# Performance work log

Measured on AMD Instinct MI355X. Metric: run time of the kernel, lower is better.

Reference implementation:

```python
import jax, jax.numpy as jnp
import numpy as np

EPS = 1e-5
NEG_SLOPE = 0.01  # torch leaky_relu default


def _layer_norm(x, g, b):
    m = jnp.mean(x, axis=-1, keepdims=True)
    v = jnp.var(x, axis=-1, keepdims=True)
    return (x - m) * jax.lax.rsqrt(v + EPS) * g + b


def setup_inputs() -> dict:
    key = jax.random.key(0)
    ks = jax.random.split(key, 8)
    bs, n, c, out_c, enc_dim = 8, 2048, 128, 128, 64
    s = 1.0 / np.sqrt(c)
    return {
        "x": jax.random.normal(ks[0], (bs, n, c), jnp.float32),
        "enc": jax.random.normal(ks[1], (bs, n, enc_dim), jnp.float32),
        "W_enc": jax.random.uniform(ks[2], (c, enc_dim), jnp.float32, -1, 1) / np.sqrt(enc_dim),
        "b_enc": jnp.zeros((c,), jnp.float32),
        "g1": jnp.ones((c,), jnp.float32),
        "b1": jnp.zeros((c,), jnp.float32),
        "g2": jnp.ones((c,), jnp.float32),
        "b2": jnp.zeros((c,), jnp.float32),
        "W0": jax.random.uniform(ks[3], (c, c), jnp.float32, -1, 1) * s,
        "Wa": jax.random.uniform(ks[4], (2 * c,), jnp.float32, -1, 1) / np.sqrt(2 * c),
        "W1": jax.random.uniform(ks[5], (out_c, c), jnp.float32, -1, 1) * s,
    }


def reference(x, enc, W_enc, b_enc, g1, b1, g2, b2, W0, Wa, W1):
    c = x.shape[-1]
    k = 1
    # positional encoding projection
    x = x + enc @ W_enc.T + b_enc
    x_norm = _layer_norm(x, g1, b1)
    # head i=0 (k=1)
    h = x_norm @ W0.T  # [bs, n, c]
    # GAT attention: e[b,i,j] = leaky_relu(a . cat(h_i, h_j)) computed via split weights
    a1, a2 = Wa[:c], Wa[c:]
    s1 = h @ a1  # [bs, n] contribution of node i
    s2 = h @ a2  # [bs, n] contribution of node j
    e = jax.nn.leaky_relu(s1[:, :, None] + s2[:, None, :], NEG_SLOPE)  # [bs, n, n]
    atten = jax.nn.softmax(e, axis=2)
    attentioned = jnp.einsum("bij,bjc->bic", atten, h)
    attentioned = attentioned + x  # residual
    attentioned = _layer_norm(attentioned, g2, b2)
    h_next = jax.nn.elu(attentioned @ W1.T) / k
    atten_agg = jax.lax.stop_gradient(atten) / k
    return h_next, atten_agg
```

## Files before the change

### kernel.cpp

```cpp
#include <hip/hip_runtime.h>
#include <hip/hip_bf16.h>
#include <cstddef>

#define EPS 1e-5f
#define NSLOPE 0.01f
#define L2E 1.44269504f

typedef __attribute__((ext_vector_type(8))) short s16x8;
typedef __attribute__((ext_vector_type(4))) float f32x4;

union BF8 { unsigned short u[8]; s16x8 v; };

static __device__ inline unsigned short f2bf(float f) {
    unsigned int u = __float_as_uint(f);
    u += 0x7fffu + ((u >> 16) & 1u);
    return (unsigned short)(u >> 16);
}

static __device__ inline void nt_store4(float* p, f32x4 v) {
    __builtin_nontemporal_store(v, (f32x4*)p);
}

__global__ __launch_bounds__(256) void kW(
    const float* __restrict__ W_enc, const float* __restrict__ W0,
    const float* __restrict__ W1,
    unsigned short* __restrict__ Web, unsigned short* __restrict__ W0b,
    unsigned short* __restrict__ W1b)
{
    int idx = blockIdx.x * 256 + threadIdx.x;
    if (idx < 128 * 64) Web[idx] = f2bf(W_enc[idx]);
    if (idx < 128 * 128) { W0b[idx] = f2bf(W0[idx]); W1b[idx] = f2bf(W1[idx]); }
}

__global__ __launch_bounds__(256, 4) void kA(
    const float* __restrict__ x, const float* __restrict__ enc,
    const unsigned short* __restrict__ Web, const float* __restrict__ b_enc,
    const float* __restrict__ g1, const float* __restrict__ b1,
    const unsigned short* __restrict__ W0b, const float* __restrict__ Wa,
    float* __restrict__ xnew, unsigned short* __restrict__ hP,
    float* __restrict__ s1, float* __restrict__ s2)
{
    __shared__ float ys[32][132];
    __shared__ unsigned short xnb[32][136];
    __shared__ unsigned short hts[128][40];
    __shared__ float ps1[2][32], ps2[2][32];

    int t = threadIdx.x;
    int w = t >> 6, lane = t & 63;
    int ml = lane & 15, quad = lane >> 4;
    int mrow = (w & 1) * 16;
    int chalf = (w >> 1) * 64;
    long long R0 = (long long)blockIdx.x * 32;
    int b = (int)(R0 >> 11);
    int jt = (int)((R0 & 2047) >> 5);

    f32x4 acc1[4] = {};
    const float* encrow = enc + (R0 + mrow + ml) * 64 + quad * 8;
#pragma unroll
    for (int kb = 0; kb < 2; ++kb) {
        float4 e0 = *(const float4*)(encrow + kb * 32);
        float4 e1 = *(const float4*)(encrow + kb * 32 + 4);
        BF8 af;
        af.u[0] = f2bf(e0.x); af.u[1] = f2bf(e0.y);
        af.u[2] = f2bf(e0.z); af.u[3] = f2bf(e0.w);
        af.u[4] = f2bf(e1.x); af.u[5] = f2bf(e1.y);
        af.u[6] = f2bf(e1.z); af.u[7] = f2bf(e1.w);
#pragma unroll
        for (int ct = 0; ct < 4; ++ct) {
            int n = chalf + ct * 16 + ml;
            s16x8 bf = *(const s16x8*)(Web + n * 64 + kb * 32 + quad * 8);
            acc1[ct] = __builtin_amdgcn_mfma_f32_16x16x32_bf16(af.v, bf, acc1[ct], 0, 0, 0);
        }
    }
#pragma unroll
    for (int ct = 0; ct < 4; ++ct) {
        int col = chalf + ct * 16 + ml;
        float be = b_enc[col];
#pragma unroll
        for (int rg = 0; rg < 4; ++rg) {
            int rl = mrow + quad * 4 + rg;
            long long row = R0 + rl;
            float y = acc1[ct][rg] + x[row * 128 + col] + be;
            xnew[row * 128 + col] = y;
            ys[rl][col] = y;
        }
    }
    __syncthreads();

    {
        int rl = t >> 3, sub = t & 7;
        float v[16];
        float s = 0.f, q = 0.f;
#pragma unroll
        for (int i = 0; i < 16; ++i) {
            v[i] = ys[rl][sub * 16 + i];
            s += v[i]; q += v[i] * v[i];
        }
#pragma unroll
        for (int m = 1; m < 8; m <<= 1) { s += __shfl_xor(s, m); q += __shfl_xor(q, m); }
        float mean = s * (1.f / 128.f);
        float var = q * (1.f / 128.f) - mean * mean;
        float rstd = rsqrtf(var + EPS);
#pragma unroll
        for (int i = 0; i < 16; ++i) {
            int col = sub * 16 + i;
            float xn = (v[i] - mean) * rstd * g1[col] + b1[col];
            xnb[rl][col] = f2bf(xn);
        }
    }
    __syncthreads();

    f32x4 acc2[4] = {};
#pragma unroll
    for (int kb = 0; kb < 4; ++kb) {
        s16x8 af = *(const s16x8*)(&xnb[mrow + ml][kb * 32 + quad * 8]);
#pragma unroll
        for (int ct = 0; ct < 4; ++ct) {
            int n = chalf + ct * 16 + ml;
            s16x8 bf = *(const s16x8*)(W0b + n * 128 + kb * 32 + quad * 8);
            acc2[ct] = __builtin_amdgcn_mfma_f32_16x16x32_bf16(af, bf, acc2[ct], 0, 0, 0);
        }
    }

#pragma unroll
    for (int ct = 0; ct < 4; ++ct) {
        int col = chalf + ct * 16 + ml;
#pragma unroll
        for (int rg = 0; rg < 4; ++rg)
            hts[col][mrow + quad * 4 + rg] = f2bf(acc2[ct][rg]);
    }
#pragma unroll
    for (int rg = 0; rg < 4; ++rg) {
        float p1 = 0.f, p2 = 0.f;
#pragma unroll
        for (int ct = 0; ct < 4; ++ct) {
            int col = chalf + ct * 16 + ml;
            p1 += acc2[ct][rg] * Wa[col];
            p2 += acc2[ct][rg] * Wa[128 + col];
        }
#pragma unroll
        for (int m = 1; m < 16; m <<= 1) { p1 += __shfl_xor(p1, m); p2 += __shfl_xor(p2, m); }
        if (ml == 0) {
            int rl = mrow + quad * 4 + rg;
            ps1[w >> 1][rl] = p1;
            ps2[w >> 1][rl] = p2;
        }
    }
    __syncthreads();
    if (t < 32) {
        s1[R0 + t] = ps1[0][t] + ps1[1][t];
        s2[R0 + t] = ps2[0][t] + ps2[1][t];
    }
    {
        int c = t >> 1, half = t & 1;
        unsigned short* dst = hP + (((long long)b * 64 + jt) * 128 + c) * 32 + half * 16;
        const unsigned short* srcp = &hts[c][half * 16];
        *(s16x8*)(dst) = *(const s16x8*)(srcp);
        *(s16x8*)(dst + 8) = *(const s16x8*)(srcp + 8);
    }
}

__global__ __launch_bounds__(1024) void kC(
    const float* __restrict__ s1, const float* __restrict__ s2,
    float* __restrict__ Crow)
{
    __shared__ float t[2048], ph[2048], pl[2048];
    __shared__ float wmax[16];
    __shared__ float M2sh;
    int tid = threadIdx.x;
    int b = blockIdx.x;
    const float* s2b = s2 + b * 2048;

    float m = -1e30f;
    for (int i = tid; i < 2048; i += 1024) {
        float v = s2b[i];
        t[i] = v;
        m = fmaxf(m, v);
    }
#pragma unroll
    for (int d = 32; d; d >>= 1) m = fmaxf(m, __shfl_xor(m, d));
    if ((tid & 63) == 0) wmax[tid >> 6] = m;
    __syncthreads();
    if (tid == 0) {
        float mm = wmax[0];
#pragma unroll
        for (int i = 1; i < 16; ++i) mm = fmaxf(mm, wmax[i]);
        M2sh = mm;
    }
    __syncthreads();
    float M2 = M2sh;

    for (int k = 2; k <= 2048; k <<= 1) {
        for (int j = k >> 1; j > 0; j >>= 1) {
            for (int i = tid; i < 2048; i += 1024) {
                int ixj = i ^ j;
                if (ixj > i) {
                    float a = t[i], c = t[ixj];
                    bool up = ((i & k) == 0);
                    if ((a > c) == up) { t[i] = c; t[ixj] = a; }
                }
            }
            __syncthreads();
        }
    }

    if (tid < 64) {
        int base = tid * 32;
        float ch = 0.f, cl = 0.f;
        for (int q = 0; q < 32; ++q) {
            float d = t[base + q] - M2;
            ch += __expf(d);           ph[base + q] = ch;
            cl += __expf(NSLOPE * d);  pl[base + q] = cl;
        }
        float sh = ch, sl = cl;
#pragma unroll
        for (int d = 1; d < 64; d <<= 1) {
            float uh = __shfl_up(sh, d);
            float ul = __shfl_up(sl, d);
            if (tid >= d) { sh += uh; sl += ul; }
        }
        float offh = sh - ch, offl = sl - cl;
        for (int q = 0; q < 32; ++q) { ph[base + q] += offh; pl[base + q] += offl; }
    }
    __syncthreads();

    float tot_hi = ph[2047];
    for (int r = tid; r < 2048; r += 1024) {
        float s1i = s1[b * 2048 + r];
        float zc = -s1i;
        int lo = 0, hi = 2048;
#pragma unroll
        for (int it = 0; it < 11; ++it) {
            int mid = (lo + hi) >> 1;
            if (t[mid] < zc) lo = mid + 1; else hi = mid;
        }
        float sum_hi = tot_hi - (lo > 0 ? ph[lo - 1] : 0.f);
        float sum_lo = (lo > 0 ? pl[lo - 1] : 0.f);
        float z0 = s1i + M2;
        float mi = fmaxf(z0, NSLOPE * z0);
        float A = __expf(z0 - mi);
        float B = __expf(NSLOPE * z0 - mi);
        Crow[b * 2048 + r] = mi + __logf(A * sum_hi + B * sum_lo);
    }
}

__global__ __launch_bounds__(256, 4) void kD(
    const float* __restrict__ s1, const float* __restrict__ s2,
    const float* __restrict__ Crow, const unsigned short* __restrict__ hP,
    float* __restrict__ atten, float* __restrict__ attn)
{
    __shared__ float Pt[4][16][36];
    __shared__ float Rbuf[3][16][132];

    int t = threadIdx.x;
    int w = t >> 6, lane = t & 63;
    int bid = blockIdx.x;
    int swz = (bid & 7) * 128 + (bid >> 3);
    int b = swz >> 7;
    int it = swz & 127;
    int i0 = it * 16;
    int ml = lane & 15, quad = lane >> 4;

    const float* s2b = s2 + (long long)b * 2048;

    float s1i  = s1[(long long)b * 2048 + i0 + ml];
    float CiL2 = Crow[(long long)b * 2048 + i0 + ml] * L2E;
    const unsigned short* hPb = hP + (long long)b * 64 * 128 * 32;
    int sr = lane >> 3, sc = lane & 7;
    float* abase = atten + ((long long)b * 2048 + i0) * 2048;

    f32x4 acc[8] = {};
    for (int jj = 0; jj < 512; jj += 32) {
        int j0 = w * 512 + jj;
        int jb = j0 + quad * 8;
        float4 sa = *(const float4*)(s2b + jb);
        float4 sb = *(const float4*)(s2b + jb + 4);
        float zs[8] = {sa.x, sa.y, sa.z, sa.w, sb.x, sb.y, sb.z, sb.w};
        float p[8];
        BF8 af;
#pragma unroll
        for (int k = 0; k < 8; ++k) {
            float z = s1i + zs[k];
            float zl = fmaxf(z, NSLOPE * z);
            p[k] = exp2f(fmaf(zl, L2E, -CiL2));
            af.u[k] = f2bf(p[k]);
        }
        *(f32x4*)&Pt[w][ml][quad * 8]     = *(const f32x4*)&p[0];
        *(f32x4*)&Pt[w][ml][quad * 8 + 4] = *(const f32x4*)&p[4];
        f32x4 r0 = *(const f32x4*)&Pt[w][sr][sc * 4];
        f32x4 r1 = *(const f32x4*)&Pt[w][8 + sr][sc * 4];
        nt_store4(abase + (long long)sr * 2048 + j0 + sc * 4, r0);
        nt_store4(abase + (long long)(8 + sr) * 2048 + j0 + sc * 4, r1);

        const unsigned short* tb = hPb + (long long)(j0 >> 5) * 128 * 32;
#pragma unroll
        for (int ct = 0; ct < 8; ++ct) {
            s16x8 bfrag = *(const s16x8*)(tb + (ct * 16 + ml) * 32 + quad * 8);
            acc[ct] = __builtin_amdgcn_mfma_f32_16x16x32_bf16(af.v, bfrag, acc[ct], 0, 0, 0);
        }
    }

    if (w > 0) {
#pragma unroll
        for (int ct = 0; ct < 8; ++ct)
#pragma unroll
            for (int rg = 0; rg < 4; ++rg)
                Rbuf[w - 1][quad * 4 + rg][ct * 16 + ml] = acc[ct][rg];
    }
    __syncthreads();
    if (w == 0) {
#pragma unroll
        for (int ct = 0; ct < 8; ++ct) {
#pragma unroll
            for (int rg = 0; rg < 4; ++rg) {
                int ii = quad * 4 + rg;
                int cc = ct * 16 + ml;
                float v = acc[ct][rg] + Rbuf[0][ii][cc] + Rbuf[1][ii][cc]
                        + Rbuf[2][ii][cc];
                attn[((long long)b * 2048 + i0 + ii) * 128 + cc] = v;
            }
        }
    }
}

__global__ __launch_bounds__(256, 4) void kE(
    const float* __restrict__ xnew, const float* __restrict__ g2,
    const float* __restrict__ b2, const unsigned short* __restrict__ W1b,
    float* __restrict__ io)
{
    __shared__ unsigned short xnb[32][136];
    int t = threadIdx.x;
    long long R0 = (long long)blockIdx.x * 32;

    {
        int rl = t >> 3, sub = t & 7;
        long long row = R0 + rl;
        const float* pio = io + row * 128 + sub * 16;
        const float* pxn = xnew + row * 128 + sub * 16;
        float v[16];
        float s = 0.f, q = 0.f;
#pragma unroll
        for (int i = 0; i < 16; i += 4) {
            float4 a = *(const float4*)(pio + i);
            float4 c = *(const float4*)(pxn + i);
            v[i]     = a.x + c.x; v[i + 1] = a.y + c.y;
            v[i + 2] = a.z + c.z; v[i + 3] = a.w + c.w;
        }
#pragma unroll
        for (int i = 0; i < 16; ++i) { s += v[i]; q += v[i] * v[i]; }
#pragma unroll
        for (int m = 1; m < 8; m <<= 1) { s += __shfl_xor(s, m); q += __shfl_xor(q, m); }
        float mean = s * (1.f / 128.f);
        float var = q * (1.f / 128.f) - mean * mean;
        float rstd = rsqrtf(var + EPS);
#pragma unroll
        for (int i = 0; i < 16; ++i) {
            int col = sub * 16 + i;
            float xn = (v[i] - mean) * rstd * g2[col] + b2[col];
            xnb[rl][col] = f2bf(xn);
        }
    }
    __syncthreads();

    int w = t >> 6, lane = t & 63;
    int ml = lane & 15, quad = lane >> 4;
    int mrow = (w & 1) * 16;
    int chalf = (w >> 1) * 64;

    f32x4 acc[4] = {};
#pragma unroll
    for (int kb = 0; kb < 4; ++kb) {
        s16x8 af = *(const s16x8*)(&xnb[mrow + ml][kb * 32 + quad * 8]);
#pragma unroll
        for (int ct = 0; ct < 4; ++ct) {
            int n = chalf + ct * 16 + ml;
            s16x8 bf = *(const s16x8*)(W1b + n * 128 + kb * 32 + quad * 8);
            acc[ct] = __builtin_amdgcn_mfma_f32_16x16x32_bf16(af, bf, acc[ct], 0, 0, 0);
        }
    }
#pragma unroll
    for (int ct = 0; ct < 4; ++ct) {
        int col = chalf + ct * 16 + ml;
#pragma unroll
        for (int rg = 0; rg < 4; ++rg) {
            int rl = mrow + quad * 4 + rg;
            float h = acc[ct][rg];
            float o = h > 0.f ? h : (__expf(h) - 1.f);
            __builtin_nontemporal_store(o, &io[(R0 + rl) * 128 + col]);
        }
    }
}

extern "C" void kernel_launch(void* const* d_in, const int* in_sizes, int n_in,
                              void* d_out, int out_size, void* d_ws, size_t ws_size,
                              hipStream_t stream)
{
    const float* x     = (const float*)d_in[0];
    const float* enc   = (const float*)d_in[1];
    const float* W_enc = (const float*)d_in[2];
    const float* b_enc = (const float*)d_in[3];
    const float* g1    = (const float*)d_in[4];
    const float* b1    = (const float*)d_in[5];
    const float* g2    = (const float*)d_in[6];
    const float* b2    = (const float*)d_in[7];
    const float* W0    = (const float*)d_in[8];
    const float* Wa    = (const float*)d_in[9];
    const float* W1    = (const float*)d_in[10];

    float* out = (float*)d_out;
    const long long ROWS = 8LL * 2048;
    const long long HN   = ROWS * 128;

    float* xnew = (float*)d_ws;
    float* s1   = xnew + HN;
    float* s2   = s1 + ROWS;
    unsigned short* hP  = (unsigned short*)(s2 + ROWS);
    unsigned short* Web = hP + HN;
    unsigned short* W0b = Web + 128 * 64;
    unsigned short* W1b = W0b + 128 * 128;
    float* Crow = (float*)(W1b + 128 * 128);

    float* atten = out + HN;
    float* attn  = out;

    kW<<<64, 256, 0, stream>>>(W_enc, W0, W1, Web, W0b, W1b);
    kA<<<512, 256, 0, stream>>>(x, enc, Web, b_enc, g1, b1, W0b, Wa,
                                xnew, hP, s1, s2);
    kC<<<8, 1024, 0, stream>>>(s1, s2, Crow);
    kD<<<1024, 256, 0, stream>>>(s1, s2, Crow, hP, atten, attn);
    kE<<<512, 256, 0, stream>>>(xnew, g2, b2, W1b, out);
}
```

Before: 244.2 us.

## Fuse softmax normalizer and final layernorm/projection into attention kernel

Drops the separate kC kernel, which used an 8-block bitonic sort plus prefix sums to get per-row log-sum-exp. Each kD block now computes its 16 rows' normalizers directly by scanning all 2048 s2 values. The kE kernel (residual, layernorm, W1 matmul, ELU) is also folded into kD's epilogue, so wave 0 does it for the block's 16 rows. This removes two launches, a low-parallelism serial kernel and an fp32 round trip of the attention output, at the cost of about 2048 extra exp evaluations per row in every block and a serialized epilogue on a single wave.

After: 220.3 us. -9.8%, faster.

```diff
diff --git a/kernel.cpp b/kernel.cpp
--- a/kernel.cpp
+++ b/kernel.cpp
@@ -160,97 +160,16 @@
     }
 }
 
-__global__ __launch_bounds__(1024) void kC(
-    const float* __restrict__ s1, const float* __restrict__ s2,
-    float* __restrict__ Crow)
-{
-    __shared__ float t[2048], ph[2048], pl[2048];
-    __shared__ float wmax[16];
-    __shared__ float M2sh;
-    int tid = threadIdx.x;
-    int b = blockIdx.x;
-    const float* s2b = s2 + b * 2048;
-
-    float m = -1e30f;
-    for (int i = tid; i < 2048; i += 1024) {
-        float v = s2b[i];
-        t[i] = v;
-        m = fmaxf(m, v);
-    }
-#pragma unroll
-    for (int d = 32; d; d >>= 1) m = fmaxf(m, __shfl_xor(m, d));
-    if ((tid & 63) == 0) wmax[tid >> 6] = m;
-    __syncthreads();
-    if (tid == 0) {
-        float mm = wmax[0];
-#pragma unroll
-        for (int i = 1; i < 16; ++i) mm = fmaxf(mm, wmax[i]);
-        M2sh = mm;
-    }
-    __syncthreads();
-    float M2 = M2sh;
-
-    for (int k = 2; k <= 2048; k <<= 1) {
-        for (int j = k >> 1; j > 0; j >>= 1) {
-            for (int i = tid; i < 2048; i += 1024) {
-                int ixj = i ^ j;
-                if (ixj > i) {
-                    float a = t[i], c = t[ixj];
-                    bool up = ((i & k) == 0);
-                    if ((a > c) == up) { t[i] = c; t[ixj] = a; }
-                }
-            }
-            __syncthreads();
-        }
-    }
-
-    if (tid < 64) {
-        int base = tid * 32;
-        float ch = 0.f, cl = 0.f;
-        for (int q = 0; q < 32; ++q) {
-            float d = t[base + q] - M2;
-            ch += __expf(d);           ph[base + q] = ch;
-            cl += __expf(NSLOPE * d);  pl[base + q] = cl;
-        }
-        float sh = ch, sl = cl;
-#pragma unroll
-        for (int d = 1; d < 64; d <<= 1) {
-            float uh = __shfl_up(sh, d);
-            float ul = __shfl_up(sl, d);
-            if (tid >= d) { sh += uh; sl += ul; }
-        }
-        float offh = sh - ch, offl = sl - cl;
-        for (int q = 0; q < 32; ++q) { ph[base + q] += offh; pl[base + q] += offl; }
-    }
-    __syncthreads();
-
-    float tot_hi = ph[2047];
-    for (int r = tid; r < 2048; r += 1024) {
-        float s1i = s1[b * 2048 + r];
-        float zc = -s1i;
-        int lo = 0, hi = 2048;
-#pragma unroll
-        for (int it = 0; it < 11; ++it) {
-            int mid = (lo + hi) >> 1;
-            if (t[mid] < zc) lo = mid + 1; else hi = mid;
-        }
-        float sum_hi = tot_hi - (lo > 0 ? ph[lo - 1] : 0.f);
-        float sum_lo = (lo > 0 ? pl[lo - 1] : 0.f);
-        float z0 = s1i + M2;
-        float mi = fmaxf(z0, NSLOPE * z0);
-        float A = __expf(z0 - mi);
-        float B = __expf(NSLOPE * z0 - mi);
-        Crow[b * 2048 + r] = mi + __logf(A * sum_hi + B * sum_lo);
-    }
-}
-
 __global__ __launch_bounds__(256, 4) void kD(
     const float* __restrict__ s1, const float* __restrict__ s2,
-    const float* __restrict__ Crow, const unsigned short* __restrict__ hP,
-    float* __restrict__ atten, float* __restrict__ attn)
+    const unsigned short* __restrict__ hP, const float* __restrict__ xnew,
+    const float* __restrict__ g2, const float* __restrict__ b2,
+    const unsigned short* __restrict__ W1b,
+    float* __restrict__ atten, float* __restrict__ out)
 {
     __shared__ float Pt[4][16][36];
     __shared__ float Rbuf[3][16][132];
+    __shared__ float s1sh[16], Csh[16];
 
     int t = threadIdx.x;
     int w = t >> 6, lane = t & 63;
@@ -263,8 +182,50 @@
 
     const float* s2b = s2 + (long long)b * 2048;
 
-    float s1i  = s1[(long long)b * 2048 + i0 + ml];
-    float CiL2 = Crow[(long long)b * 2048 + i0 + ml] * L2E;
+    float mxs = -1e30f;
+    for (int j = lane * 4; j < 2048; j += 256) {
+        float4 v = *(const float4*)(s2b + j);
+        mxs = fmaxf(fmaxf(mxs, fmaxf(v.x, v.y)), fmaxf(v.z, v.w));
+    }
+#pragma unroll
+    for (int m = 32; m; m >>= 1) mxs = fmaxf(mxs, __shfl_xor(mxs, m));
+
+    float s1r[4], mi[4], miL2[4], li[4];
+#pragma unroll
+    for (int r = 0; r < 4; ++r) {
+        s1r[r] = s1[(long long)b * 2048 + i0 + w * 4 + r];
+        float z0 = s1r[r] + mxs;
+        mi[r] = fmaxf(z0, NSLOPE * z0);
+        miL2[r] = mi[r] * L2E;
+        li[r] = 0.f;
+    }
+    for (int j = lane * 4; j < 2048; j += 256) {
+        float4 v = *(const float4*)(s2b + j);
+        float vv[4] = {v.x, v.y, v.z, v.w};
+#pragma unroll
+        for (int r = 0; r < 4; ++r) {
+#pragma unroll
+            for (int k = 0; k < 4; ++k) {
+                float z = s1r[r] + vv[k];
+                float zl = fmaxf(z, NSLOPE * z);
+                li[r] += exp2f(fmaf(zl, L2E, -miL2[r]));
+            }
+        }
+    }
+#pragma unroll
+    for (int r = 0; r < 4; ++r) {
+        float l = li[r];
+#pragma unroll
+        for (int m = 32; m; m >>= 1) l += __shfl_xor(l, m);
+        if (lane == 0) {
+            s1sh[w * 4 + r] = s1r[r];
+            Csh[w * 4 + r] = mi[r] + __logf(l);
+        }
+    }
+    __syncthreads();
+
+    float s1i = s1sh[ml];
+    float CiL2 = Csh[ml] * L2E;
     const unsigned short* hPb = hP + (long long)b * 64 * 128 * 32;
     int sr = lane >> 3, sc = lane & 7;
     float* abase = atten + ((long long)b * 2048 + i0) * 2048;
@@ -308,85 +269,66 @@
                 Rbuf[w - 1][quad * 4 + rg][ct * 16 + ml] = acc[ct][rg];
     }
     __syncthreads();
-    if (w == 0) {
+    if (w > 0) return;
+
+    const float* xrow = xnew + ((long long)b * 2048 + i0) * 128;
+    float v[8][4];
+#pragma unroll
+    for (int ct = 0; ct < 8; ++ct) {
+#pragma unroll
+        for (int rg = 0; rg < 4; ++rg) {
+            int ii = quad * 4 + rg;
+            int cc = ct * 16 + ml;
+            v[ct][rg] = acc[ct][rg] + Rbuf[0][ii][cc] + Rbuf[1][ii][cc]
+                      + Rbuf[2][ii][cc] + xrow[ii * 128 + cc];
+        }
+    }
+    float sm[4] = {}, qm[4] = {};
+#pragma unroll
+    for (int ct = 0; ct < 8; ++ct)
+#pragma unroll
+        for (int rg = 0; rg < 4; ++rg) { sm[rg] += v[ct][rg]; qm[rg] += v[ct][rg] * v[ct][rg]; }
+#pragma unroll
+    for (int rg = 0; rg < 4; ++rg) {
+#pragma unroll
+        for (int m = 1; m < 16; m <<= 1) {
+            sm[rg] += __shfl_xor(sm[rg], m);
+            qm[rg] += __shfl_xor(qm[rg], m);
+        }
+    }
+    unsigned short* xnb2 = (unsigned short*)&Pt[0][0][0];
+#pragma unroll
+    for (int rg = 0; rg < 4; ++rg) {
+        float mean = sm[rg] * (1.f / 128.f);
+        float var = qm[rg] * (1.f / 128.f) - mean * mean;
+        float rstd = rsqrtf(var + EPS);
+        int ii = quad * 4 + rg;
 #pragma unroll
         for (int ct = 0; ct < 8; ++ct) {
-#pragma unroll
-            for (int rg = 0; rg < 4; ++rg) {
-                int ii = quad * 4 + rg;
-                int cc = ct * 16 + ml;
-                float v = acc[ct][rg] + Rbuf[0][ii][cc] + Rbuf[1][ii][cc]
-                        + Rbuf[2][ii][cc];
-                attn[((long long)b * 2048 + i0 + ii) * 128 + cc] = v;
-            }
-        }
-    }
-}
-
-__global__ __launch_bounds__(256, 4) void kE(
-    const float* __restrict__ xnew, const float* __restrict__ g2,
-    const float* __restrict__ b2, const unsigned short* __restrict__ W1b,
-    float* __restrict__ io)
-{
-    __shared__ unsigned short xnb[32][136];
-    int t = threadIdx.x;
-    long long R0 = (long long)blockIdx.x * 32;
-
-    {
-        int rl = t >> 3, sub = t & 7;
-        long long row = R0 + rl;
-        const float* pio = io + row * 128 + sub * 16;
-        const float* pxn = xnew + row * 128 + sub * 16;
-        float v[16];
-        float s = 0.f, q = 0.f;
-#pragma unroll
-        for (int i = 0; i < 16; i += 4) {
-            float4 a = *(const float4*)(pio + i);
-            float4 c = *(const float4*)(pxn + i);
-            v[i]     = a.x + c.x; v[i + 1] = a.y + c.y;
-            v[i + 2] = a.z + c.z; v[i + 3] = a.w + c.w;
-        }
-#pragma unroll
-        for (int i = 0; i < 16; ++i) { s += v[i]; q += v[i] * v[i]; }
-#pragma unroll
-        for (int m = 1; m < 8; m <<= 1) { s += __shfl_xor(s, m); q += __shfl_xor(q, m); }
-        float mean = s * (1.f / 128.f);
-        float var = q * (1.f / 128.f) - mean * mean;
-        float rstd = rsqrtf(var + EPS);
-#pragma unroll
-        for (int i = 0; i < 16; ++i) {
-            int col = sub * 16 + i;
-            float xn = (v[i] - mean) * rstd * g2[col] + b2[col];
-            xnb[rl][col] = f2bf(xn);
-        }
-    }
-    __syncthreads();
-
-    int w = t >> 6, lane = t & 63;
-    int ml = lane & 15, quad = lane >> 4;
-    int mrow = (w & 1) * 16;
-    int chalf = (w >> 1) * 64;
-
-    f32x4 acc[4] = {};
+            int cc = ct * 16 + ml;
+            float xn = (v[ct][rg] - mean) * rstd * g2[cc] + b2[cc];
+            xnb2[ii * 136 + cc] = f2bf(xn);
+        }
+    }
+    f32x4 acc2[8] = {};
 #pragma unroll
     for (int kb = 0; kb < 4; ++kb) {
-        s16x8 af = *(const s16x8*)(&xnb[mrow + ml][kb * 32 + quad * 8]);
-#pragma unroll
-        for (int ct = 0; ct < 4; ++ct) {
-            int n = chalf + ct * 16 + ml;
-            s16x8 bf = *(const s16x8*)(W1b + n * 128 + kb * 32 + quad * 8);
-            acc[ct] = __builtin_amdgcn_mfma_f32_16x16x32_bf16(af, bf, acc[ct], 0, 0, 0);
-        }
-    }
-#pragma unroll
-    for (int ct = 0; ct < 4; ++ct) {
-        int col = chalf + ct * 16 + ml;
+        s16x8 af = *(const s16x8*)(xnb2 + ml * 136 + kb * 32 + quad * 8);
+#pragma unroll
+        for (int ct = 0; ct < 8; ++ct) {
+            s16x8 bf = *(const s16x8*)(W1b + (ct * 16 + ml) * 128 + kb * 32 + quad * 8);
+            acc2[ct] = __builtin_amdgcn_mfma_f32_16x16x32_bf16(af, bf, acc2[ct], 0, 0, 0);
+        }
+    }
+#pragma unroll
+    for (int ct = 0; ct < 8; ++ct) {
 #pragma unroll
         for (int rg = 0; rg < 4; ++rg) {
-            int rl = mrow + quad * 4 + rg;
-            float h = acc[ct][rg];
+            int ii = quad * 4 + rg;
+            int cc = ct * 16 + ml;
+            float h = acc2[ct][rg];
             float o = h > 0.f ? h : (__expf(h) - 1.f);
-            __builtin_nontemporal_store(o, &io[(R0 + rl) * 128 + col]);
+            __builtin_nontemporal_store(o, &out[((long long)b * 2048 + i0 + ii) * 128 + cc]);
         }
     }
 }
@@ -418,15 +360,11 @@
     unsigned short* Web = hP + HN;
     unsigned short* W0b = Web + 128 * 64;
     unsigned short* W1b = W0b + 128 * 128;
-    float* Crow = (float*)(W1b + 128 * 128);
 
     float* atten = out + HN;
-    float* attn  = out;
 
     kW<<<64, 256, 0, stream>>>(W_enc, W0, W1, Web, W0b, W1b);
     kA<<<512, 256, 0, stream>>>(x, enc, Web, b_enc, g1, b1, W0b, Wa,
                                 xnew, hP, s1, s2);
-    kC<<<8, 1024, 0, stream>>>(s1, s2, Crow);
-    kD<<<1024, 256, 0, stream>>>(s1, s2, Crow, hP, atten, attn);
-    kE<<<512, 256, 0, stream>>>(xnew, g2, b2, W1b, out);
-}
+    kD<<<1024, 256, 0, stream>>>(s1, s2, hP, xnew, g2, b2, W1b, atten, out);
+}
```
